# Performance work log

Measured on AMD Instinct MI355X. Metric: run time of the kernel, lower is better.

The kernel has to match this reference:

```python
import jax, jax.numpy as jnp
import numpy as np

B, S, E, H = 64, 256, 512, 1024  # batch, seq_len, embed, hidden (dis_size=[512,1024,1024])


def _ln(x, g, b, eps=1e-5):
    # LayerNorm over last axis; x: [..., 3, H], g/b: [3, H] (per-gate affine)
    m = x.mean(-1, keepdims=True)
    v = ((x - m) ** 2).mean(-1, keepdims=True)
    return (x - m) * jax.lax.rsqrt(v + eps) * g + b


def _gru_cell(h, x, Wih, Whh, bih, bhh, gig, gib, ghg, ghb):
    Bsz = x.shape[0]
    Hh = h.shape[1]
    pi = _ln((x @ Wih.T + bih).reshape(Bsz, 3, Hh), gig, gib)
    ph = _ln((h @ Whh.T + bhh).reshape(Bsz, 3, Hh), ghg, ghb)
    r = jax.nn.sigmoid(pi[:, 0] + ph[:, 0])
    z = jax.nn.sigmoid(pi[:, 1] + ph[:, 1])
    n = jnp.tanh(pi[:, 2] + r * ph[:, 2])
    return (1.0 - z) * n + z * h


def _unroll(x, layers, W_out, b_out):
    # x: [B, S, E] -> scalar score per batch element from last hidden state
    xs = jnp.swapaxes(x, 0, 1)  # [S, B, E]
    for (Wih, Whh, bih, bhh, gig, gib, ghg, ghb) in layers:
        h0 = jnp.zeros((x.shape[0], Whh.shape[1]), x.dtype)

        def step(h, xt, Wih=Wih, Whh=Whh, bih=bih, bhh=bhh, gig=gig, gib=gib, ghg=ghg, ghb=ghb):
            h2 = _gru_cell(h, xt, Wih, Whh, bih, bhh, gig, gib, ghg, ghb)
            return h2, h2

        _, xs = jax.lax.scan(step, h0, xs)  # xs becomes [S, B, H]
    return (xs[-1] @ W_out.T + b_out)[:, 0]  # [B]


def setup_inputs() -> dict:
    key = jax.random.key(0)
    ks = jax.random.split(key, 12)
    sizes = [(E, H), (H, H)]  # (input_size, hidden_size) per layer
    inp = {
        "generated_data": jax.random.normal(ks[0], (B, S, E), jnp.float32),
        "true_data": jax.random.normal(ks[1], (B, S, E), jnp.float32),
    }
    for li, (ins, hs) in enumerate(sizes):
        k = jax.random.split(ks[2 + li], 4)
        inp[f"W_ih{li}"] = jax.random.normal(k[0], (3 * hs, ins), jnp.float32) * 0.02
        inp[f"W_hh{li}"] = jax.random.normal(k[1], (3 * hs, hs), jnp.float32) * 0.02
        inp[f"b_ih{li}"] = jnp.zeros((3 * hs,), jnp.float32)
        inp[f"b_hh{li}"] = jnp.zeros((3 * hs,), jnp.float32)
        inp[f"gi_g{li}"] = jnp.ones((3, hs), jnp.float32)
        inp[f"gi_b{li}"] = jnp.zeros((3, hs), jnp.float32)
        inp[f"gh_g{li}"] = jnp.ones((3, hs), jnp.float32)
        inp[f"gh_b{li}"] = jnp.zeros((3, hs), jnp.float32)
    inp["W_out"] = jax.random.normal(ks[10], (1, H), jnp.float32) * 0.02
    inp["b_out"] = jnp.zeros((1,), jnp.float32)
    return inp


def reference(generated_data, true_data,
              W_ih0, W_hh0, b_ih0, b_hh0, gi_g0, gi_b0, gh_g0, gh_b0,
              W_ih1, W_hh1, b_ih1, b_hh1, gi_g1, gi_b1, gh_g1, gh_b1,
              W_out, b_out):
    layers = [
        (W_ih0, W_hh0, b_ih0, b_hh0, gi_g0, gi_b0, gh_g0, gh_b0),
        (W_ih1, W_hh1, b_ih1, b_hh1, gi_g1, gi_b1, gh_g1, gh_b1),
    ]
    true_labels = _unroll(true_data, layers, W_out, b_out)
    gen_labels = _unroll(generated_data, layers, W_out, b_out)
    discriminator_loss = -true_labels.mean() + gen_labels.mean()
    generator_loss = -gen_labels.mean()
    return (discriminator_loss, generator_loss)
```

## Files before the change

kernel.cpp:

```cpp
#include <hip/hip_runtime.h>
#include <math.h>

#define NCH   128
#define SLEN  256
#define HDIM  1024
#define N3    3072

typedef __attribute__((ext_vector_type(8))) __bf16 bf16x8;
typedef __attribute__((ext_vector_type(4))) float  f32x4;

__device__ __forceinline__ f32x4 mfma_bf16(bf16x8 a, bf16x8 b, f32x4 c) {
  return __builtin_amdgcn_mfma_f32_16x16x32_bf16(a, b, c, 0, 0, 0);
}

__device__ __forceinline__ float ld_sc1_f32(const float* p) {
  return __hip_atomic_load(p, __ATOMIC_RELAXED, __HIP_MEMORY_SCOPE_AGENT);
}
__device__ __forceinline__ void st_sc1_f32(float* p, float v) {
  __hip_atomic_store(p, v, __ATOMIC_RELAXED, __HIP_MEMORY_SCOPE_AGENT);
}
__device__ __forceinline__ unsigned long long ld_sc1_u64(const unsigned long long* p) {
  return __hip_atomic_load(p, __ATOMIC_RELAXED, __HIP_MEMORY_SCOPE_AGENT);
}
__device__ __forceinline__ void st_sc1_u32(unsigned int* p, unsigned int v) {
  __hip_atomic_store(p, v, __ATOMIC_RELAXED, __HIP_MEMORY_SCOPE_AGENT);
}
__device__ __forceinline__ int ld_sc1_i32(const int* p) {
  return __hip_atomic_load(p, __ATOMIC_RELAXED, __HIP_MEMORY_SCOPE_AGENT);
}
__device__ __forceinline__ void st_sc1_i32(int* p, int v) {
  __hip_atomic_store(p, v, __ATOMIC_RELAXED, __HIP_MEMORY_SCOPE_AGENT);
}

__global__ void split_w(const float* __restrict__ src, __bf16* __restrict__ dh,
                        __bf16* __restrict__ dl, int n)
{
  int i = blockIdx.x * blockDim.x + threadIdx.x;
  if (i < n) {
    float x = src[i];
    __bf16 h = (__bf16)x;
    float r = x - (float)h;
    dh[i] = h;
    dl[i] = (__bf16)r;
  }
}

__global__ void zero_kernel(float* __restrict__ p, int n)
{
  int i = blockIdx.x * blockDim.x + threadIdx.x;
  if (i < n) p[i] = 0.f;
}

__global__ __launch_bounds__(256) void xproj_mfma(
    const float* __restrict__ A0, const float* __restrict__ A1,
    int chainsA0, int strideChain, int t0, int K, int lTc,
    const __bf16* __restrict__ Wh, const __bf16* __restrict__ Wl,
    const float* __restrict__ bias, float* __restrict__ out)
{
  __shared__ __bf16 Ah[4][128][8];
  __shared__ __bf16 Al[4][128][8];
  const int tid  = threadIdx.x;
  const int n0   = blockIdx.x * 128;
  const int row0 = blockIdx.y * 128;
  const int lane = tid & 63;
  const int wv   = tid >> 6;
  const int q    = lane >> 4;
  const int c15  = lane & 15;
  const int m_off = wv * 32;
  const int sr  = tid >> 1;
  const int sq0 = (tid & 1) * 2;
  const int sk  = (tid & 1) * 16;
  const int r     = row0 + sr;
  const int chain = r >> lTc;
  const int dt    = r & ((1 << lTc) - 1);
  const float* aptr = (chain < chainsA0)
      ? (A0 + ((size_t)chain * strideChain + t0 + dt) * K)
      : (A1 + ((size_t)(chain - chainsA0) * strideChain + t0 + dt) * K);

  f32x4 acc[2][8];
#pragma unroll
  for (int i = 0; i < 2; ++i)
#pragma unroll
    for (int j = 0; j < 8; ++j) acc[i][j] = (f32x4){0.f, 0.f, 0.f, 0.f};

  for (int k0 = 0; k0 < K; k0 += 32) {
    float f[16];
    *(float4*)(f + 0)  = *(const float4*)(aptr + k0 + sk + 0);
    *(float4*)(f + 4)  = *(const float4*)(aptr + k0 + sk + 4);
    *(float4*)(f + 8)  = *(const float4*)(aptr + k0 + sk + 8);
    *(float4*)(f + 12) = *(const float4*)(aptr + k0 + sk + 12);
    bf16x8 hv0, hv1, lv0, lv1;
#pragma unroll
    for (int e = 0; e < 8; ++e) {
      __bf16 h0 = (__bf16)f[e];
      hv0[e] = h0;  lv0[e] = (__bf16)(f[e] - (float)h0);
      __bf16 h1 = (__bf16)f[8 + e];
      hv1[e] = h1;  lv1[e] = (__bf16)(f[8 + e] - (float)h1);
    }
    __syncthreads();
    *(bf16x8*)&Ah[sq0][sr][0]     = hv0;
    *(bf16x8*)&Ah[sq0 + 1][sr][0] = hv1;
    *(bf16x8*)&Al[sq0][sr][0]     = lv0;
    *(bf16x8*)&Al[sq0 + 1][sr][0] = lv1;
    __syncthreads();

    bf16x8 a_h[2], a_l[2];
#pragma unroll
    for (int i = 0; i < 2; ++i) {
      a_h[i] = *(const bf16x8*)&Ah[q][m_off + i * 16 + c15][0];
      a_l[i] = *(const bf16x8*)&Al[q][m_off + i * 16 + c15][0];
    }
#pragma unroll
    for (int j = 0; j < 8; ++j) {
      const size_t woff = (size_t)(n0 + j * 16 + c15) * K + k0 + q * 8;
      bf16x8 b_h = *(const bf16x8*)(Wh + woff);
      bf16x8 b_l = *(const bf16x8*)(Wl + woff);
#pragma unroll
      for (int i = 0; i < 2; ++i) {
        acc[i][j] = mfma_bf16(a_h[i], b_h, acc[i][j]);
        acc[i][j] = mfma_bf16(a_h[i], b_l, acc[i][j]);
        acc[i][j] = mfma_bf16(a_l[i], b_h, acc[i][j]);
      }
    }
  }

#pragma unroll
  for (int j = 0; j < 8; ++j) {
    const int col = n0 + j * 16 + c15;
    const float bcol = bias[col];
#pragma unroll
    for (int i = 0; i < 2; ++i) {
#pragma unroll
      for (int rr = 0; rr < 4; ++rr) {
        const int m = m_off + i * 16 + q * 4 + rr;
        out[(size_t)(row0 + m) * N3 + col] = acc[i][j][rr] + bcol;
      }
    }
  }
}

__global__ __launch_bounds__(256) void ln_rows(float* __restrict__ a,
    const float* __restrict__ gw, const float* __restrict__ gb)
{
  const int row = blockIdx.x;
  const int g   = blockIdx.y;
  const int tid = threadIdx.x;
  float* base = a + (size_t)row * N3 + g * 1024;
  __shared__ float redS[4], redS2[4];
  __shared__ float s_mean, s_rstd;
  const int j = tid * 4;
  float4 v = *(const float4*)(base + j);
  float s  = v.x + v.y + v.z + v.w;
  float s2 = v.x*v.x + v.y*v.y + v.z*v.z + v.w*v.w;
#pragma unroll
  for (int off = 32; off > 0; off >>= 1) {
    s  += __shfl_down(s, off);
    s2 += __shfl_down(s2, off);
  }
  if ((tid & 63) == 0) { redS[tid >> 6] = s; redS2[tid >> 6] = s2; }
  __syncthreads();
  if (tid == 0) {
    float S  = redS[0] + redS[1] + redS[2] + redS[3];
    float S2 = redS2[0] + redS2[1] + redS2[2] + redS2[3];
    float mean = S * (1.f / 1024.f);
    float var  = S2 * (1.f / 1024.f) - mean * mean;
    s_mean = mean;
    s_rstd = rsqrtf(var + 1e-5f);
  }
  __syncthreads();
  float mean = s_mean, rstd = s_rstd;
  float4 gwv = *(const float4*)(gw + g * 1024 + j);
  float4 gbv = *(const float4*)(gb + g * 1024 + j);
  float4 o;
  o.x = (v.x - mean) * rstd * gwv.x + gbv.x;
  o.y = (v.y - mean) * rstd * gwv.y + gbv.y;
  o.z = (v.z - mean) * rstd * gwv.z + gbv.z;
  o.w = (v.w - mean) * rstd * gwv.w + gbv.w;
  *(float4*)(base + j) = o;
}

__global__ __launch_bounds__(512, 2) void recur_pers(
    const __bf16* __restrict__ Wh, const __bf16* __restrict__ Wl,
    const float* __restrict__ bhh,
    const float* __restrict__ ghw, const float* __restrict__ ghb,
    const float* __restrict__ pi,
    unsigned int* __restrict__ Hpk,
    float* __restrict__ h_carry,
    float* __restrict__ hseq,
    float* __restrict__ stats_part,
    int* __restrict__ flag_a, int* __restrict__ flag_b,
    int Tc, int firstChunk)
{
  const int tid  = threadIdx.x;
  const int bid  = blockIdx.x;
  const int gid  = bid >> 5;
  const int ct   = bid & 31;
  const int lane = tid & 63;
  const int w    = tid >> 6;
  const int q    = lane >> 4;
  const int c15  = lane & 15;
  const int m    = tid & 15;
  const int col  = tid >> 4;
  const int ch   = gid * 16 + m;
  const int Hcol = ct * 32 + col;

  __shared__ float red[8 * 6 * 16 * 20];
  __shared__ float sred[8 * 16 * 6];
  __shared__ float sstat[96];

  bf16x8 bh[6][4], bl[6][4];
  const int kw = w * 128;
#pragma unroll
  for (int t = 0; t < 6; ++t) {
    const int gate = t >> 1, half = t & 1;
    const size_t nrow = (size_t)(gate * 1024 + ct * 32 + half * 16 + c15);
#pragma unroll
    for (int kc = 0; kc < 4; ++kc) {
      const size_t off = nrow * HDIM + kw + kc * 32 + q * 8;
      bh[t][kc] = *(const bf16x8*)(Wh + off);
      bl[t][kc] = *(const bf16x8*)(Wl + off);
    }
  }

  const float bias0 = bhh[Hcol], bias1 = bhh[1024 + Hcol], bias2 = bhh[2048 + Hcol];
  const float lw0 = ghw[Hcol], lw1 = ghw[1024 + Hcol], lw2 = ghw[2048 + Hcol];
  const float lb0 = ghb[Hcol], lb1 = ghb[1024 + Hcol], lb2 = ghb[2048 + Hcol];
  float hprev = firstChunk ? 0.f : h_carry[(size_t)ch * HDIM + Hcol];

  const size_t arowbase = (size_t)(gid * 16 + c15) * HDIM;
  float* my_part = stats_part + ((size_t)gid * 32 + ct) * 96;
  const int* fA = flag_a + (gid << 5);
  const int* fB = flag_b + (gid << 5);
  const int pidx = lane & 31;

  for (int dt = 0; dt < Tc; ++dt) {
    const float* pirow = pi + ((size_t)ch * Tc + dt) * N3 + Hcol;
    const float pr = pirow[0], pz = pirow[1024], pn = pirow[2048];

    if (w == 0 && dt > 0) {
      while (true) {
        int v = ld_sc1_i32(fB + pidx);
        if (!__any(v < dt)) break;
        __builtin_amdgcn_s_sleep(1);
      }
    }
    __syncthreads();
    __asm__ __volatile__("" ::: "memory");

    f32x4 acc[6];
#pragma unroll
    for (int t = 0; t < 6; ++t) acc[t] = (f32x4){0.f, 0.f, 0.f, 0.f};

    unsigned long long abuf[2][4];
#pragma unroll
    for (int j = 0; j < 4; ++j) {
      abuf[0][j] = ld_sc1_u64((const unsigned long long*)(Hpk + arowbase + kw + 0 * 32 + q * 8) + j);
      abuf[1][j] = ld_sc1_u64((const unsigned long long*)(Hpk + arowbase + kw + 1 * 32 + q * 8) + j);
    }
#pragma unroll
    for (int kc = 0; kc < 4; ++kc) {
      unsigned int u[8];
#pragma unroll
      for (int j = 0; j < 4; ++j) {
        u[2 * j]     = (unsigned int)(abuf[kc & 1][j]);
        u[2 * j + 1] = (unsigned int)(abuf[kc & 1][j] >> 32);
      }
      union { unsigned int d[4]; bf16x8 v; } uah, ual;
#pragma unroll
      for (int d = 0; d < 4; ++d) {
        uah.d[d] = __builtin_amdgcn_perm(u[2 * d + 1], u[2 * d], 0x05040100u);
        ual.d[d] = __builtin_amdgcn_perm(u[2 * d + 1], u[2 * d], 0x07060302u);
      }
      if (kc < 2) {
#pragma unroll
        for (int j = 0; j < 4; ++j)
          abuf[kc & 1][j] = ld_sc1_u64(
              (const unsigned long long*)(Hpk + arowbase + kw + (kc + 2) * 32 + q * 8) + j);
      }
      bf16x8 ah = uah.v, al = ual.v;
#pragma unroll
      for (int t = 0; t < 6; ++t) {
        acc[t] = mfma_bf16(ah, bh[t][kc], acc[t]);
        acc[t] = mfma_bf16(ah, bl[t][kc], acc[t]);
        acc[t] = mfma_bf16(al, bh[t][kc], acc[t]);
      }
    }

#pragma unroll
    for (int t = 0; t < 6; ++t) {
      const int idx = ((w * 6 + t) * 16 + c15) * 20 + q * 4;
      *(f32x4*)&red[idx] = acc[t];
    }
    __syncthreads();

    float phv0 = 0.f, phv1 = 0.f, phv2 = 0.f;
    {
      const int cn = col & 15;
      const int hi = col >> 4;
#pragma unroll
      for (int w8 = 0; w8 < 8; ++w8) {
        phv0 += red[((w8 * 6 + 0 * 2 + hi) * 16 + cn) * 20 + m];
        phv1 += red[((w8 * 6 + 1 * 2 + hi) * 16 + cn) * 20 + m];
        phv2 += red[((w8 * 6 + 2 * 2 + hi) * 16 + cn) * 20 + m];
      }
    }
    phv0 += bias0; phv1 += bias1; phv2 += bias2;

    {
      float s0 = phv0, s1 = phv1, s2 = phv2;
      float q0 = phv0 * phv0, q1 = phv1 * phv1, q2 = phv2 * phv2;
#pragma unroll
      for (int mm = 16; mm <= 32; mm <<= 1) {
        s0 += __shfl_xor(s0, mm); q0 += __shfl_xor(q0, mm);
        s1 += __shfl_xor(s1, mm); q1 += __shfl_xor(q1, mm);
        s2 += __shfl_xor(s2, mm); q2 += __shfl_xor(q2, mm);
      }
      if (lane < 16) {
        const int b = (w * 16 + lane) * 6;
        sred[b + 0] = s0; sred[b + 1] = q0;
        sred[b + 2] = s1; sred[b + 3] = q1;
        sred[b + 4] = s2; sred[b + 5] = q2;
      }
    }
    __syncthreads();

    if (tid < 96) {
      const int m6 = tid / 6;
      const int r6 = tid - m6 * 6;
      float v = 0.f;
#pragma unroll
      for (int w8 = 0; w8 < 8; ++w8) v += sred[(w8 * 16 + m6) * 6 + r6];
      st_sc1_f32(&my_part[tid], v);
    }
    __syncthreads();
    if (tid == 0) st_sc1_i32((int*)fA + ct, dt + 1);

    if (w == 0) {
      while (true) {
        int v = ld_sc1_i32(fA + pidx);
        if (!__any(v < dt + 1)) break;
        __builtin_amdgcn_s_sleep(1);
      }
    }
    __syncthreads();
    __asm__ __volatile__("" ::: "memory");

    {
      const int cidx = tid >> 4;
      const float* sp = stats_part + ((size_t)gid * 32 + cidx) * 96 + m * 6;
      float p0 = ld_sc1_f32(sp + 0), p1 = ld_sc1_f32(sp + 1), p2 = ld_sc1_f32(sp + 2);
      float p3 = ld_sc1_f32(sp + 3), p4 = ld_sc1_f32(sp + 4), p5 = ld_sc1_f32(sp + 5);
      p0 += __shfl_xor(p0, 16); p1 += __shfl_xor(p1, 16); p2 += __shfl_xor(p2, 16);
      p3 += __shfl_xor(p3, 16); p4 += __shfl_xor(p4, 16); p5 += __shfl_xor(p5, 16);
      p0 += __shfl_xor(p0, 32); p1 += __shfl_xor(p1, 32); p2 += __shfl_xor(p2, 32);
      p3 += __shfl_xor(p3, 32); p4 += __shfl_xor(p4, 32); p5 += __shfl_xor(p5, 32);
      if (lane < 16) {
        const int b = w * 104 + lane * 6;
        red[b + 0] = p0; red[b + 1] = p1; red[b + 2] = p2;
        red[b + 3] = p3; red[b + 4] = p4; red[b + 5] = p5;
      }
    }
    __syncthreads();
    if (tid < 96) {
      float v = 0.f;
#pragma unroll
      for (int w8 = 0; w8 < 8; ++w8) v += red[w8 * 104 + tid];
      sstat[tid] = v;
    }
    __syncthreads();

    {
      const int b = m * 6;
      const float mean0 = sstat[b + 0] * (1.f / 1024.f);
      const float var0  = sstat[b + 1] * (1.f / 1024.f) - mean0 * mean0;
      const float mean1 = sstat[b + 2] * (1.f / 1024.f);
      const float var1  = sstat[b + 3] * (1.f / 1024.f) - mean1 * mean1;
      const float mean2 = sstat[b + 4] * (1.f / 1024.f);
      const float var2  = sstat[b + 5] * (1.f / 1024.f) - mean2 * mean2;
      const float nh0 = (phv0 - mean0) * rsqrtf(var0 + 1e-5f) * lw0 + lb0;
      const float nh1 = (phv1 - mean1) * rsqrtf(var1 + 1e-5f) * lw1 + lb1;
      const float nh2 = (phv2 - mean2) * rsqrtf(var2 + 1e-5f) * lw2 + lb2;
      const float r  = 1.f / (1.f + expf(-(pr + nh0)));
      const float z  = 1.f / (1.f + expf(-(pz + nh1)));
      const float nn = tanhf(pn + r * nh2);
      const float hn = (1.f - z) * nn + z * hprev;
      hprev = hn;
      const __bf16 hb = (__bf16)hn;
      const __bf16 lo = (__bf16)(hn - (float)hb);
      unsigned short hs, ls;
      __builtin_memcpy(&hs, &hb, 2);
      __builtin_memcpy(&ls, &lo, 2);
      st_sc1_u32(Hpk + (size_t)ch * HDIM + Hcol,
                 (unsigned int)hs | ((unsigned int)ls << 16));
      if (hseq) hseq[((size_t)ch * Tc + dt) * HDIM + Hcol] = hn;
      if (dt == Tc - 1) h_carry[(size_t)ch * HDIM + Hcol] = hn;
    }
    __syncthreads();
    if (tid == 0) st_sc1_i32((int*)fB + ct, dt + 1);
  }
}

__global__ __launch_bounds__(256) void label_kernel(const float* __restrict__ h,
    const float* __restrict__ Wout, const float* __restrict__ bout,
    float* __restrict__ labels)
{
  const int c = blockIdx.x;
  const int tid = threadIdx.x;
  __shared__ float red[4];
  float4 hv = *(const float4*)(h + (size_t)c * HDIM + tid * 4);
  float4 wv = *(const float4*)(Wout + tid * 4);
  float s = hv.x * wv.x + hv.y * wv.y + hv.z * wv.z + hv.w * wv.w;
#pragma unroll
  for (int off = 32; off > 0; off >>= 1) s += __shfl_down(s, off);
  if ((tid & 63) == 0) red[tid >> 6] = s;
  __syncthreads();
  if (tid == 0) labels[c] = red[0] + red[1] + red[2] + red[3] + bout[0];
}

__global__ void loss_kernel(const float* __restrict__ labels, float* __restrict__ out)
{
  const int tid = threadIdx.x;
  __shared__ float rg[2], rt[2];
  float v = labels[tid];
  float g = (tid < 64) ? v : 0.f;
  float t = (tid >= 64) ? v : 0.f;
#pragma unroll
  for (int off = 32; off > 0; off >>= 1) {
    g += __shfl_down(g, off);
    t += __shfl_down(t, off);
  }
  if ((tid & 63) == 0) { rg[tid >> 6] = g; rt[tid >> 6] = t; }
  __syncthreads();
  if (tid == 0) {
    float gm = (rg[0] + rg[1]) * (1.f / 64.f);
    float tm = (rt[0] + rt[1]) * (1.f / 64.f);
    out[0] = -tm + gm;
    out[1] = -gm;
  }
}

extern "C" void kernel_launch(void* const* d_in, const int* in_sizes, int n_in,
                              void* d_out, int out_size, void* d_ws, size_t ws_size,
                              hipStream_t stream)
{
  const float* gen  = (const float*)d_in[0];
  const float* tru  = (const float*)d_in[1];
  const float* Wih0 = (const float*)d_in[2];
  const float* Whh0 = (const float*)d_in[3];
  const float* bih0 = (const float*)d_in[4];
  const float* bhh0 = (const float*)d_in[5];
  const float* gig0 = (const float*)d_in[6];
  const float* gib0 = (const float*)d_in[7];
  const float* ghg0 = (const float*)d_in[8];
  const float* ghb0 = (const float*)d_in[9];
  const float* Wih1 = (const float*)d_in[10];
  const float* Whh1 = (const float*)d_in[11];
  const float* bih1 = (const float*)d_in[12];
  const float* bhh1 = (const float*)d_in[13];
  const float* gig1 = (const float*)d_in[14];
  const float* gib1 = (const float*)d_in[15];
  const float* ghg1 = (const float*)d_in[16];
  const float* ghb1 = (const float*)d_in[17];
  const float* Wout = (const float*)d_in[18];
  const float* bout = (const float*)d_in[19];
  float* out = (float*)d_out;

  __bf16* bp = (__bf16*)d_ws;
  __bf16* Whh0h = bp;  bp += (size_t)N3 * HDIM;
  __bf16* Whh0l = bp;  bp += (size_t)N3 * HDIM;
  __bf16* Whh1h = bp;  bp += (size_t)N3 * HDIM;
  __bf16* Whh1l = bp;  bp += (size_t)N3 * HDIM;
  __bf16* Wih1h = bp;  bp += (size_t)N3 * HDIM;
  __bf16* Wih1l = bp;  bp += (size_t)N3 * HDIM;
  __bf16* Wih0h = bp;  bp += (size_t)N3 * 512;
  __bf16* Wih0l = bp;  bp += (size_t)N3 * 512;
  unsigned int* H0pk = (unsigned int*)bp;
  unsigned int* H1pk = H0pk + (size_t)NCH * HDIM;
  const size_t bf16Bytes = ((char*)(H1pk + (size_t)NCH * HDIM)) - (char*)d_ws;

  const size_t fixedF = 2 * (size_t)NCH * HDIM + 256 + 8 * 32 * 96 + 1024;
  int Tc = 256;
  while (Tc > 1) {
    size_t needF = (size_t)NCH * Tc * (N3 + HDIM) + fixedF;
    if (bf16Bytes + needF * 4 <= ws_size) break;
    Tc >>= 1;
  }
  int lTc = 0;
  while ((1 << lTc) < Tc) ++lTc;

  float* fp       = (float*)((char*)d_ws + bf16Bytes);
  float* pi_chunk = fp;   fp += (size_t)NCH * Tc * N3;
  float* h0_chunk = fp;   fp += (size_t)NCH * Tc * HDIM;
  float* h_cur0   = fp;   fp += (size_t)NCH * HDIM;
  float* h_cur1   = fp;   fp += (size_t)NCH * HDIM;
  float* labels   = fp;   fp += 256;
  float* stats    = fp;   fp += 8 * 32 * 96;
  int*   flag_a   = (int*)fp;
  int*   flag_b   = flag_a + 256;

  {
    const int nW = N3 * HDIM;
    split_w<<<(nW + 255) / 256, 256, 0, stream>>>(Whh0, Whh0h, Whh0l, nW);
    split_w<<<(nW + 255) / 256, 256, 0, stream>>>(Whh1, Whh1h, Whh1l, nW);
    split_w<<<(nW + 255) / 256, 256, 0, stream>>>(Wih1, Wih1h, Wih1l, nW);
    const int nW0 = N3 * 512;
    split_w<<<(nW0 + 255) / 256, 256, 0, stream>>>(Wih0, Wih0h, Wih0l, nW0);
  }
  zero_kernel<<<(2 * NCH * HDIM) / 256, 256, 0, stream>>>((float*)H0pk, 2 * NCH * HDIM);

  const int nChunks = SLEN / Tc;
  for (int cidx = 0; cidx < nChunks; ++cidx) {
    const int t0 = cidx * Tc;
    const int first = (cidx == 0) ? 1 : 0;
    xproj_mfma<<<dim3(24, Tc), 256, 0, stream>>>(
        gen, tru, 64, SLEN, t0, 512, lTc, Wih0h, Wih0l, bih0, pi_chunk);
    ln_rows<<<dim3(NCH * Tc, 3), 256, 0, stream>>>(pi_chunk, gig0, gib0);
    zero_kernel<<<2, 256, 0, stream>>>((float*)flag_a, 512);
    recur_pers<<<256, 512, 0, stream>>>(
        Whh0h, Whh0l, bhh0, ghg0, ghb0, pi_chunk, H0pk, h_cur0,
        h0_chunk, stats, flag_a, flag_b, Tc, first);
    xproj_mfma<<<dim3(24, Tc), 256, 0, stream>>>(
        h0_chunk, h0_chunk, NCH, Tc, 0, 1024, lTc, Wih1h, Wih1l, bih1, pi_chunk);
    ln_rows<<<dim3(NCH * Tc, 3), 256, 0, stream>>>(pi_chunk, gig1, gib1);
    zero_kernel<<<2, 256, 0, stream>>>((float*)flag_a, 512);
    recur_pers<<<256, 512, 0, stream>>>(
        Whh1h, Whh1l, bhh1, ghg1, ghb1, pi_chunk, H1pk, h_cur1,
        (float*)nullptr, stats, flag_a, flag_b, Tc, first);
  }

  label_kernel<<<NCH, 256, 0, stream>>>(h_cur1, Wout, bout, labels);
  loss_kernel<<<1, 128, 0, stream>>>(labels, out);
}
```

Measured before the change: 9.400 ms.

## Fuse input-gate LayerNorm into recurrent kernel and merge prep/readout launches

```diff
diff --git a/kernel.cpp b/kernel.cpp
--- a/kernel.cpp
+++ b/kernel.cpp
@@ -32,23 +32,33 @@
   __hip_atomic_store(p, v, __ATOMIC_RELAXED, __HIP_MEMORY_SCOPE_AGENT);
 }
 
-__global__ void split_w(const float* __restrict__ src, __bf16* __restrict__ dh,
-                        __bf16* __restrict__ dl, int n)
+__global__ __launch_bounds__(256) void prep(
+    const float* __restrict__ Whh0, const float* __restrict__ Whh1,
+    const float* __restrict__ Wih1, const float* __restrict__ Wih0,
+    __bf16* __restrict__ Whh0h, __bf16* __restrict__ Whh0l,
+    __bf16* __restrict__ Whh1h, __bf16* __restrict__ Whh1l,
+    __bf16* __restrict__ Wih1h, __bf16* __restrict__ Wih1l,
+    __bf16* __restrict__ Wih0h, __bf16* __restrict__ Wih0l,
+    unsigned int* __restrict__ Hpk,
+    int* __restrict__ flags)
 {
-  int i = blockIdx.x * blockDim.x + threadIdx.x;
-  if (i < n) {
-    float x = src[i];
-    __bf16 h = (__bf16)x;
-    float r = x - (float)h;
-    dh[i] = h;
-    dl[i] = (__bf16)r;
-  }
-}
-
-__global__ void zero_kernel(float* __restrict__ p, int n)
-{
-  int i = blockIdx.x * blockDim.x + threadIdx.x;
-  if (i < n) p[i] = 0.f;
+  const int NB = N3 * HDIM;
+  const int NS = N3 * 512;
+  int i = blockIdx.x * 256 + threadIdx.x;
+  const float* src; __bf16 *dh, *dl; int j;
+  if (i < NB)            { src = Whh0; dh = Whh0h; dl = Whh0l; j = i; }
+  else if (i < 2 * NB)   { src = Whh1; dh = Whh1h; dl = Whh1l; j = i - NB; }
+  else if (i < 3 * NB)   { src = Wih1; dh = Wih1h; dl = Wih1l; j = i - 2 * NB; }
+  else if (i < 3 * NB + NS) { src = Wih0; dh = Wih0h; dl = Wih0l; j = i - 3 * NB; }
+  else if (i < 3 * NB + NS + 2 * NCH * HDIM) { Hpk[i - 3 * NB - NS] = 0u; return; }
+  else if (i < 3 * NB + NS + 2 * NCH * HDIM + 512) {
+    flags[i - 3 * NB - NS - 2 * NCH * HDIM] = 0; return;
+  }
+  else return;
+  float x = src[j];
+  __bf16 h = (__bf16)x;
+  dh[j] = h;
+  dl[j] = (__bf16)(x - (float)h);
 }
 
 __global__ __launch_bounds__(256) void xproj_mfma(
@@ -139,57 +149,18 @@
   }
 }
 
-__global__ __launch_bounds__(256) void ln_rows(float* __restrict__ a,
-    const float* __restrict__ gw, const float* __restrict__ gb)
-{
-  const int row = blockIdx.x;
-  const int g   = blockIdx.y;
-  const int tid = threadIdx.x;
-  float* base = a + (size_t)row * N3 + g * 1024;
-  __shared__ float redS[4], redS2[4];
-  __shared__ float s_mean, s_rstd;
-  const int j = tid * 4;
-  float4 v = *(const float4*)(base + j);
-  float s  = v.x + v.y + v.z + v.w;
-  float s2 = v.x*v.x + v.y*v.y + v.z*v.z + v.w*v.w;
-#pragma unroll
-  for (int off = 32; off > 0; off >>= 1) {
-    s  += __shfl_down(s, off);
-    s2 += __shfl_down(s2, off);
-  }
-  if ((tid & 63) == 0) { redS[tid >> 6] = s; redS2[tid >> 6] = s2; }
-  __syncthreads();
-  if (tid == 0) {
-    float S  = redS[0] + redS[1] + redS[2] + redS[3];
-    float S2 = redS2[0] + redS2[1] + redS2[2] + redS2[3];
-    float mean = S * (1.f / 1024.f);
-    float var  = S2 * (1.f / 1024.f) - mean * mean;
-    s_mean = mean;
-    s_rstd = rsqrtf(var + 1e-5f);
-  }
-  __syncthreads();
-  float mean = s_mean, rstd = s_rstd;
-  float4 gwv = *(const float4*)(gw + g * 1024 + j);
-  float4 gbv = *(const float4*)(gb + g * 1024 + j);
-  float4 o;
-  o.x = (v.x - mean) * rstd * gwv.x + gbv.x;
-  o.y = (v.y - mean) * rstd * gwv.y + gbv.y;
-  o.z = (v.z - mean) * rstd * gwv.z + gbv.z;
-  o.w = (v.w - mean) * rstd * gwv.w + gbv.w;
-  *(float4*)(base + j) = o;
-}
-
 __global__ __launch_bounds__(512, 2) void recur_pers(
     const __bf16* __restrict__ Wh, const __bf16* __restrict__ Wl,
     const float* __restrict__ bhh,
     const float* __restrict__ ghw, const float* __restrict__ ghb,
+    const float* __restrict__ giw, const float* __restrict__ gib,
     const float* __restrict__ pi,
     unsigned int* __restrict__ Hpk,
     float* __restrict__ h_carry,
     float* __restrict__ hseq,
     float* __restrict__ stats_part,
     int* __restrict__ flag_a, int* __restrict__ flag_b,
-    int Tc, int firstChunk)
+    int Tc, int firstChunk, int base)
 {
   const int tid  = threadIdx.x;
   const int bid  = blockIdx.x;
@@ -204,9 +175,9 @@
   const int ch   = gid * 16 + m;
   const int Hcol = ct * 32 + col;
 
-  __shared__ float red[8 * 6 * 16 * 20];
-  __shared__ float sred[8 * 16 * 6];
-  __shared__ float sstat[96];
+  __shared__ float red[8 * 6 * 16 * 16];
+  __shared__ float sred[8 * 16 * 12];
+  __shared__ float sstat[192];
 
   bf16x8 bh[6][4], bl[6][4];
   const int kw = w * 128;
@@ -225,10 +196,12 @@
   const float bias0 = bhh[Hcol], bias1 = bhh[1024 + Hcol], bias2 = bhh[2048 + Hcol];
   const float lw0 = ghw[Hcol], lw1 = ghw[1024 + Hcol], lw2 = ghw[2048 + Hcol];
   const float lb0 = ghb[Hcol], lb1 = ghb[1024 + Hcol], lb2 = ghb[2048 + Hcol];
+  const float iw0 = giw[Hcol], iw1 = giw[1024 + Hcol], iw2 = giw[2048 + Hcol];
+  const float ib0 = gib[Hcol], ib1 = gib[1024 + Hcol], ib2 = gib[2048 + Hcol];
   float hprev = firstChunk ? 0.f : h_carry[(size_t)ch * HDIM + Hcol];
 
   const size_t arowbase = (size_t)(gid * 16 + c15) * HDIM;
-  float* my_part = stats_part + ((size_t)gid * 32 + ct) * 96;
+  float* my_part = stats_part + ((size_t)gid * 32 + ct) * 192;
   const int* fA = flag_a + (gid << 5);
   const int* fB = flag_b + (gid << 5);
   const int pidx = lane & 31;
@@ -240,7 +213,7 @@
     if (w == 0 && dt > 0) {
       while (true) {
         int v = ld_sc1_i32(fB + pidx);
-        if (!__any(v < dt)) break;
+        if (!__any(v < base + dt)) break;
         __builtin_amdgcn_s_sleep(1);
       }
     }
@@ -288,7 +261,7 @@
 
 #pragma unroll
     for (int t = 0; t < 6; ++t) {
-      const int idx = ((w * 6 + t) * 16 + c15) * 20 + q * 4;
+      const int idx = ((w * 6 + t) * 16 + c15) * 16 + q * 4;
       *(f32x4*)&red[idx] = acc[t];
     }
     __syncthreads();
@@ -299,9 +272,9 @@
       const int hi = col >> 4;
 #pragma unroll
       for (int w8 = 0; w8 < 8; ++w8) {
-        phv0 += red[((w8 * 6 + 0 * 2 + hi) * 16 + cn) * 20 + m];
-        phv1 += red[((w8 * 6 + 1 * 2 + hi) * 16 + cn) * 20 + m];
-        phv2 += red[((w8 * 6 + 2 * 2 + hi) * 16 + cn) * 20 + m];
+        phv0 += red[((w8 * 6 + 0 * 2 + hi) * 16 + cn) * 16 + m];
+        phv1 += red[((w8 * 6 + 1 * 2 + hi) * 16 + cn) * 16 + m];
+        phv2 += red[((w8 * 6 + 2 * 2 + hi) * 16 + cn) * 16 + m];
       }
     }
     phv0 += bias0; phv1 += bias1; phv2 += bias2;
@@ -309,36 +282,44 @@
     {
       float s0 = phv0, s1 = phv1, s2 = phv2;
       float q0 = phv0 * phv0, q1 = phv1 * phv1, q2 = phv2 * phv2;
+      float s3 = pr, s4 = pz, s5 = pn;
+      float q3 = pr * pr, q4 = pz * pz, q5 = pn * pn;
 #pragma unroll
       for (int mm = 16; mm <= 32; mm <<= 1) {
         s0 += __shfl_xor(s0, mm); q0 += __shfl_xor(q0, mm);
         s1 += __shfl_xor(s1, mm); q1 += __shfl_xor(q1, mm);
         s2 += __shfl_xor(s2, mm); q2 += __shfl_xor(q2, mm);
+        s3 += __shfl_xor(s3, mm); q3 += __shfl_xor(q3, mm);
+        s4 += __shfl_xor(s4, mm); q4 += __shfl_xor(q4, mm);
+        s5 += __shfl_xor(s5, mm); q5 += __shfl_xor(q5, mm);
       }
       if (lane < 16) {
-        const int b = (w * 16 + lane) * 6;
-        sred[b + 0] = s0; sred[b + 1] = q0;
-        sred[b + 2] = s1; sred[b + 3] = q1;
-        sred[b + 4] = s2; sred[b + 5] = q2;
-      }
-    }
-    __syncthreads();
-
-    if (tid < 96) {
-      const int m6 = tid / 6;
-      const int r6 = tid - m6 * 6;
+        const int b = (w * 16 + lane) * 12;
+        sred[b + 0] = s0;  sred[b + 1] = q0;
+        sred[b + 2] = s1;  sred[b + 3] = q1;
+        sred[b + 4] = s2;  sred[b + 5] = q2;
+        sred[b + 6] = s3;  sred[b + 7] = q3;
+        sred[b + 8] = s4;  sred[b + 9] = q4;
+        sred[b + 10] = s5; sred[b + 11] = q5;
+      }
+    }
+    __syncthreads();
+
+    if (tid < 192) {
+      const int m12 = tid / 12;
+      const int r12 = tid - m12 * 12;
       float v = 0.f;
 #pragma unroll
-      for (int w8 = 0; w8 < 8; ++w8) v += sred[(w8 * 16 + m6) * 6 + r6];
+      for (int w8 = 0; w8 < 8; ++w8) v += sred[(w8 * 16 + m12) * 12 + r12];
       st_sc1_f32(&my_part[tid], v);
     }
     __syncthreads();
-    if (tid == 0) st_sc1_i32((int*)fA + ct, dt + 1);
+    if (tid == 0) st_sc1_i32((int*)fA + ct, base + dt + 1);
 
     if (w == 0) {
       while (true) {
         int v = ld_sc1_i32(fA + pidx);
-        if (!__any(v < dt + 1)) break;
+        if (!__any(v < base + dt + 1)) break;
         __builtin_amdgcn_s_sleep(1);
       }
     }
@@ -347,42 +328,59 @@
 
     {
       const int cidx = tid >> 4;
-      const float* sp = stats_part + ((size_t)gid * 32 + cidx) * 96 + m * 6;
-      float p0 = ld_sc1_f32(sp + 0), p1 = ld_sc1_f32(sp + 1), p2 = ld_sc1_f32(sp + 2);
-      float p3 = ld_sc1_f32(sp + 3), p4 = ld_sc1_f32(sp + 4), p5 = ld_sc1_f32(sp + 5);
+      const float* sp = stats_part + ((size_t)gid * 32 + cidx) * 192 + m * 12;
+      float p0 = ld_sc1_f32(sp + 0),  p1 = ld_sc1_f32(sp + 1),  p2 = ld_sc1_f32(sp + 2);
+      float p3 = ld_sc1_f32(sp + 3),  p4 = ld_sc1_f32(sp + 4),  p5 = ld_sc1_f32(sp + 5);
+      float p6 = ld_sc1_f32(sp + 6),  p7 = ld_sc1_f32(sp + 7),  p8 = ld_sc1_f32(sp + 8);
+      float p9 = ld_sc1_f32(sp + 9),  p10 = ld_sc1_f32(sp + 10), p11 = ld_sc1_f32(sp + 11);
       p0 += __shfl_xor(p0, 16); p1 += __shfl_xor(p1, 16); p2 += __shfl_xor(p2, 16);
       p3 += __shfl_xor(p3, 16); p4 += __shfl_xor(p4, 16); p5 += __shfl_xor(p5, 16);
+      p6 += __shfl_xor(p6, 16); p7 += __shfl_xor(p7, 16); p8 += __shfl_xor(p8, 16);
+      p9 += __shfl_xor(p9, 16); p10 += __shfl_xor(p10, 16); p11 += __shfl_xor(p11, 16);
       p0 += __shfl_xor(p0, 32); p1 += __shfl_xor(p1, 32); p2 += __shfl_xor(p2, 32);
       p3 += __shfl_xor(p3, 32); p4 += __shfl_xor(p4, 32); p5 += __shfl_xor(p5, 32);
+      p6 += __shfl_xor(p6, 32); p7 += __shfl_xor(p7, 32); p8 += __shfl_xor(p8, 32);
+      p9 += __shfl_xor(p9, 32); p10 += __shfl_xor(p10, 32); p11 += __shfl_xor(p11, 32);
       if (lane < 16) {
-        const int b = w * 104 + lane * 6;
-        red[b + 0] = p0; red[b + 1] = p1; red[b + 2] = p2;
-        red[b + 3] = p3; red[b + 4] = p4; red[b + 5] = p5;
-      }
-    }
-    __syncthreads();
-    if (tid < 96) {
+        const int b = w * 200 + lane * 12;
+        red[b + 0] = p0;  red[b + 1] = p1;  red[b + 2] = p2;
+        red[b + 3] = p3;  red[b + 4] = p4;  red[b + 5] = p5;
+        red[b + 6] = p6;  red[b + 7] = p7;  red[b + 8] = p8;
+        red[b + 9] = p9;  red[b + 10] = p10; red[b + 11] = p11;
+      }
+    }
+    __syncthreads();
+    if (tid < 192) {
       float v = 0.f;
 #pragma unroll
-      for (int w8 = 0; w8 < 8; ++w8) v += red[w8 * 104 + tid];
+      for (int w8 = 0; w8 < 8; ++w8) v += red[w8 * 200 + tid];
       sstat[tid] = v;
     }
     __syncthreads();
 
     {
-      const int b = m * 6;
-      const float mean0 = sstat[b + 0] * (1.f / 1024.f);
-      const float var0  = sstat[b + 1] * (1.f / 1024.f) - mean0 * mean0;
-      const float mean1 = sstat[b + 2] * (1.f / 1024.f);
-      const float var1  = sstat[b + 3] * (1.f / 1024.f) - mean1 * mean1;
-      const float mean2 = sstat[b + 4] * (1.f / 1024.f);
-      const float var2  = sstat[b + 5] * (1.f / 1024.f) - mean2 * mean2;
-      const float nh0 = (phv0 - mean0) * rsqrtf(var0 + 1e-5f) * lw0 + lb0;
-      const float nh1 = (phv1 - mean1) * rsqrtf(var1 + 1e-5f) * lw1 + lb1;
-      const float nh2 = (phv2 - mean2) * rsqrtf(var2 + 1e-5f) * lw2 + lb2;
-      const float r  = 1.f / (1.f + expf(-(pr + nh0)));
-      const float z  = 1.f / (1.f + expf(-(pz + nh1)));
-      const float nn = tanhf(pn + r * nh2);
+      const int b = m * 12;
+      const float mh0 = sstat[b + 0] * (1.f / 1024.f);
+      const float vh0 = sstat[b + 1] * (1.f / 1024.f) - mh0 * mh0;
+      const float mh1 = sstat[b + 2] * (1.f / 1024.f);
+      const float vh1 = sstat[b + 3] * (1.f / 1024.f) - mh1 * mh1;
+      const float mh2 = sstat[b + 4] * (1.f / 1024.f);
+      const float vh2 = sstat[b + 5] * (1.f / 1024.f) - mh2 * mh2;
+      const float mi0 = sstat[b + 6] * (1.f / 1024.f);
+      const float vi0 = sstat[b + 7] * (1.f / 1024.f) - mi0 * mi0;
+      const float mi1 = sstat[b + 8] * (1.f / 1024.f);
+      const float vi1 = sstat[b + 9] * (1.f / 1024.f) - mi1 * mi1;
+      const float mi2 = sstat[b + 10] * (1.f / 1024.f);
+      const float vi2 = sstat[b + 11] * (1.f / 1024.f) - mi2 * mi2;
+      const float nh0 = (phv0 - mh0) * rsqrtf(vh0 + 1e-5f) * lw0 + lb0;
+      const float nh1 = (phv1 - mh1) * rsqrtf(vh1 + 1e-5f) * lw1 + lb1;
+      const float nh2 = (phv2 - mh2) * rsqrtf(vh2 + 1e-5f) * lw2 + lb2;
+      const float ni0 = (pr - mi0) * rsqrtf(vi0 + 1e-5f) * iw0 + ib0;
+      const float ni1 = (pz - mi1) * rsqrtf(vi1 + 1e-5f) * iw1 + ib1;
+      const float ni2 = (pn - mi2) * rsqrtf(vi2 + 1e-5f) * iw2 + ib2;
+      const float r  = 1.f / (1.f + expf(-(ni0 + nh0)));
+      const float z  = 1.f / (1.f + expf(-(ni1 + nh1)));
+      const float nn = tanhf(ni2 + r * nh2);
       const float hn = (1.f - z) * nn + z * hprev;
       hprev = hn;
       const __bf16 hb = (__bf16)hn;
@@ -396,40 +394,45 @@
       if (dt == Tc - 1) h_carry[(size_t)ch * HDIM + Hcol] = hn;
     }
     __syncthreads();
-    if (tid == 0) st_sc1_i32((int*)fB + ct, dt + 1);
-  }
-}
-
-__global__ __launch_bounds__(256) void label_kernel(const float* __restrict__ h,
+    if (tid == 0) st_sc1_i32((int*)fB + ct, base + dt + 1);
+  }
+}
+
+__global__ __launch_bounds__(1024) void readout(const float* __restrict__ h,
     const float* __restrict__ Wout, const float* __restrict__ bout,
-    float* __restrict__ labels)
+    float* __restrict__ out)
 {
-  const int c = blockIdx.x;
-  const int tid = threadIdx.x;
-  __shared__ float red[4];
-  float4 hv = *(const float4*)(h + (size_t)c * HDIM + tid * 4);
-  float4 wv = *(const float4*)(Wout + tid * 4);
-  float s = hv.x * wv.x + hv.y * wv.y + hv.z * wv.z + hv.w * wv.w;
-#pragma unroll
-  for (int off = 32; off > 0; off >>= 1) s += __shfl_down(s, off);
-  if ((tid & 63) == 0) red[tid >> 6] = s;
+  const int tid  = threadIdx.x;
+  const int lane = tid & 63;
+  const int w    = tid >> 6;
+  __shared__ float lab[128];
+  __shared__ float rg[2], rt[2];
+  const int c  = w * 8 + (lane >> 3);
+  const int j0 = (lane & 7) * 128;
+  const float* hp = h + (size_t)c * HDIM + j0;
+  float s = 0.f;
+#pragma unroll
+  for (int j = 0; j < 128; j += 4) {
+    float4 v  = *(const float4*)(hp + j);
+    float4 wv = *(const float4*)(Wout + j0 + j);
+    s += v.x * wv.x + v.y * wv.y + v.z * wv.z + v.w * wv.w;
+  }
+  s += __shfl_xor(s, 1);
+  s += __shfl_xor(s, 2);
+  s += __shfl_xor(s, 4);
+  if ((lane & 7) == 0) lab[c] = s + bout[0];
   __syncthreads();
-  if (tid == 0) labels[c] = red[0] + red[1] + red[2] + red[3] + bout[0];
-}
-
-__global__ void loss_kernel(const float* __restrict__ labels, float* __restrict__ out)
-{
-  const int tid = threadIdx.x;
-  __shared__ float rg[2], rt[2];
-  float v = labels[tid];
-  float g = (tid < 64) ? v : 0.f;
-  float t = (tid >= 64) ? v : 0.f;
-#pragma unroll
-  for (int off = 32; off > 0; off >>= 1) {
-    g += __shfl_down(g, off);
-    t += __shfl_down(t, off);
-  }
-  if ((tid & 63) == 0) { rg[tid >> 6] = g; rt[tid >> 6] = t; }
+  if (tid < 128) {
+    float v = lab[tid];
+    float g = (tid < 64) ? v : 0.f;
+    float t = (tid >= 64) ? v : 0.f;
+#pragma unroll
+    for (int off = 32; off > 0; off >>= 1) {
+      g += __shfl_down(g, off);
+      t += __shfl_down(t, off);
+    }
+    if ((tid & 63) == 0) { rg[tid >> 6] = g; rt[tid >> 6] = t; }
+  }
   __syncthreads();
   if (tid == 0) {
     float gm = (rg[0] + rg[1]) * (1.f / 64.f);
@@ -478,7 +481,7 @@
   unsigned int* H1pk = H0pk + (size_t)NCH * HDIM;
   const size_t bf16Bytes = ((char*)(H1pk + (size_t)NCH * HDIM)) - (char*)d_ws;
 
-  const size_t fixedF = 2 * (size_t)NCH * HDIM + 256 + 8 * 32 * 96 + 1024;
+  const size_t fixedF = 2 * (size_t)NCH * HDIM + 8 * 32 * 192 + 1024;
   int Tc = 256;
   while (Tc > 1) {
     size_t needF = (size_t)NCH * Tc * (N3 + HDIM) + fixedF;
@@ -493,20 +496,17 @@
   float* h0_chunk = fp;   fp += (size_t)NCH * Tc * HDIM;
   float* h_cur0   = fp;   fp += (size_t)NCH * HDIM;
   float* h_cur1   = fp;   fp += (size_t)NCH * HDIM;
-  float* labels   = fp;   fp += 256;
-  float* stats    = fp;   fp += 8 * 32 * 96;
+  float* stats    = fp;   fp += 8 * 32 * 192;
   int*   flag_a   = (int*)fp;
   int*   flag_b   = flag_a + 256;
 
   {
-    const int nW = N3 * HDIM;
-    split_w<<<(nW + 255) / 256, 256, 0, stream>>>(Whh0, Whh0h, Whh0l, nW);
-    split_w<<<(nW + 255) / 256, 256, 0, stream>>>(Whh1, Whh1h, Whh1l, nW);
-    split_w<<<(nW + 255) / 256, 256, 0, stream>>>(Wih1, Wih1h, Wih1l, nW);
-    const int nW0 = N3 * 512;
-    split_w<<<(nW0 + 255) / 256, 256, 0, stream>>>(Wih0, Wih0h, Wih0l, nW0);
-  }
-  zero_kernel<<<(2 * NCH * HDIM) / 256, 256, 0, stream>>>((float*)H0pk, 2 * NCH * HDIM);
+    const int total = 3 * (N3 * HDIM) + (N3 * 512) + 2 * NCH * HDIM + 512;
+    prep<<<(total + 255) / 256, 256, 0, stream>>>(
+        Whh0, Whh1, Wih1, Wih0,
+        Whh0h, Whh0l, Whh1h, Whh1l, Wih1h, Wih1l, Wih0h, Wih0l,
+        H0pk, flag_a);
+  }
 
   const int nChunks = SLEN / Tc;
   for (int cidx = 0; cidx < nChunks; ++cidx) {
@@ -514,20 +514,15 @@
     const int first = (cidx == 0) ? 1 : 0;
     xproj_mfma<<<dim3(24, Tc), 256, 0, stream>>>(
         gen, tru, 64, SLEN, t0, 512, lTc, Wih0h, Wih0l, bih0, pi_chunk);
-    ln_rows<<<dim3(NCH * Tc, 3), 256, 0, stream>>>(pi_chunk, gig0, gib0);
-    zero_kernel<<<2, 256, 0, stream>>>((float*)flag_a, 512);
     recur_pers<<<256, 512, 0, stream>>>(
-        Whh0h, Whh0l, bhh0, ghg0, ghb0, pi_chunk, H0pk, h_cur0,
-        h0_chunk, stats, flag_a, flag_b, Tc, first);
+        Whh0h, Whh0l, bhh0, ghg0, ghb0, gig0, gib0, pi_chunk, H0pk, h_cur0,
+        h0_chunk, stats, flag_a, flag_b, Tc, first, (cidx * 2 + 0) * Tc);
     xproj_mfma<<<dim3(24, Tc), 256, 0, stream>>>(
         h0_chunk, h0_chunk, NCH, Tc, 0, 1024, lTc, Wih1h, Wih1l, bih1, pi_chunk);
-    ln_rows<<<dim3(NCH * Tc, 3), 256, 0, stream>>>(pi_chunk, gig1, gib1);
-    zero_kernel<<<2, 256, 0, stream>>>((float*)flag_a, 512);
     recur_pers<<<256, 512, 0, stream>>>(
-        Whh1h, Whh1l, bhh1, ghg1, ghb1, pi_chunk, H1pk, h_cur1,
-        (float*)nullptr, stats, flag_a, flag_b, Tc, first);
-  }
-
-  label_kernel<<<NCH, 256, 0, stream>>>(h_cur1, Wout, bout, labels);
-  loss_kernel<<<1, 128, 0, stream>>>(labels, out);
-}
+        Whh1h, Whh1l, bhh1, ghg1, ghb1, gig1, gib1, pi_chunk, H1pk, h_cur1,
+        (float*)nullptr, stats, flag_a, flag_b, Tc, first, (cidx * 2 + 1) * Tc);
+  }
+
+  readout<<<1, 1024, 0, stream>>>(h_cur1, Wout, bout, out);
+}
```

Measured after the change: 10.09 ms. 7.3% more time.
